# Performance work log

Hardware: AMD Instinct MI355X
Metric: run time of the kernel (lower is better)

The kernel has to match this reference:

```python
import jax, jax.numpy as jnp
import numpy as np

TEMP = 0.07
LAMBDA_INFONCE = 1.0
LAMBDA_NTXENT = 0.5
EPS = 1e-8

B, S, H, C = 32, 2048, 1024, 5


def _l2norm(x):
    # F.normalize-style row L2 normalization
    n = jnp.sqrt(jnp.sum(x * x, axis=1, keepdims=True))
    return x / jnp.maximum(n, 1e-12)


def _proj(x, W1, b1, W2, b2):
    h = jax.nn.relu(x @ W1 + b1)
    return _l2norm(h @ W2 + b2)


def setup_inputs() -> dict:
    key = jax.random.key(0)
    ks = jax.random.split(key, 12)
    sc1 = 1.0 / np.sqrt(H)
    sc2 = 1.0 / np.sqrt(H // 2)
    sc3 = 1.0 / np.sqrt(2 * H)
    return {
        "span_features": jax.random.normal(ks[0], (B, S, H), jnp.float32),
        "aspect_logits": jax.random.normal(ks[1], (B, S, C), jnp.float32),
        "opinion_logits": jax.random.normal(ks[2], (B, S, C), jnp.float32),
        "sentiment_labels": jax.random.randint(ks[3], (B,), 0, 3),
        "Wa1": jax.random.normal(ks[4], (H, H // 2), jnp.float32) * sc1,
        "ba1": jnp.zeros((H // 2,), jnp.float32),
        "Wa2": jax.random.normal(ks[5], (H // 2, 128), jnp.float32) * sc2,
        "ba2": jnp.zeros((128,), jnp.float32),
        "Wo1": jax.random.normal(ks[6], (H, H // 2), jnp.float32) * sc1,
        "bo1": jnp.zeros((H // 2,), jnp.float32),
        "Wo2": jax.random.normal(ks[7], (H // 2, 128), jnp.float32) * sc2,
        "bo2": jnp.zeros((128,), jnp.float32),
        "Ws1": jax.random.normal(ks[8], (2 * H, H), jnp.float32) * sc3,
        "bs1": jnp.zeros((H,), jnp.float32),
        "Ws2": jax.random.normal(ks[9], (H, 256), jnp.float32) * sc1,
        "bs2": jnp.zeros((256,), jnp.float32),
    }


def _pool(span_features, logits):
    # attention pooling: softmax over seq of summed non-O class logits
    w = jax.nn.softmax(logits[:, :, 1:].sum(axis=-1), axis=-1)  # [B, S]
    return jnp.einsum("bsh,bs->bh", span_features, w)  # [B, H]


def _infonce(a, o, labels):
    n = a.shape[0]
    sim = (a @ o.T) / TEMP  # [B, B]
    same = labels[:, None] == labels[None, :]
    eye = jnp.eye(n, dtype=a.dtype)
    pos_mask = eye + 0.5 * (same & (eye == 0)).astype(a.dtype)
    exp_sim = jnp.exp(sim)
    return -jnp.mean(jnp.log((exp_sim * pos_mask).sum(1) / exp_sim.sum(1) + EPS))


def _ntxent(s, labels):
    n = s.shape[0]
    s = _l2norm(s)
    sim = (s @ s.T) / TEMP
    same = (labels[:, None] == labels[None, :]).astype(s.dtype)
    mask = same - jnp.eye(n, dtype=s.dtype)
    exp_sim = jnp.exp(sim)
    pos = (exp_sim * mask).sum(1)
    neg = (exp_sim * (1.0 - mask)).sum(1)
    pos_count = mask.sum(1)
    has_pos = pos_count > 0
    row = jnp.where(has_pos,
                    -jnp.log(pos / (pos + neg) + EPS) / jnp.maximum(pos_count, 1.0),
                    0.0)
    return row.sum() / jnp.maximum(has_pos.sum(), 1).astype(s.dtype)


def reference(span_features, aspect_logits, opinion_logits, sentiment_labels,
              Wa1, ba1, Wa2, ba2, Wo1, bo1, Wo2, bo2, Ws1, bs1, Ws2, bs2):
    a_emb = _pool(span_features, aspect_logits)   # [B, H]
    o_emb = _pool(span_features, opinion_logits)  # [B, H]
    a_proj = _proj(a_emb, Wa1, ba1, Wa2, ba2)     # [B, 128]
    o_proj = _proj(o_emb, Wo1, bo1, Wo2, bo2)     # [B, 128]
    infonce = _infonce(a_proj, o_proj, sentiment_labels)
    s_proj = _proj(jnp.concatenate([a_emb, o_emb], axis=-1), Ws1, bs1, Ws2, bs2)
    ntxent = _ntxent(s_proj, sentiment_labels)
    # generation_embeddings is None -> cross_modal_loss = 0
    return LAMBDA_INFONCE * infonce + LAMBDA_NTXENT * ntxent
```

## Files before the change

kernel.cpp:

```cpp
#include <hip/hip_runtime.h>
#include <hip/hip_bf16.h>

#define BB 32
#define SS 2048
#define HH 1024
#define CC 5
#define TEMP_INV (1.0f/0.07f)

__global__ __launch_bounds__(256) void pool_weights(const float* __restrict__ alog,
                             const float* __restrict__ olog,
                             float* __restrict__ w_a,
                             float* __restrict__ w_o) {
    int b = blockIdx.x >> 1;
    int which = blockIdx.x & 1;
    const float* lg = which ? olog : alog;
    float* wout = which ? w_o : w_a;
    __shared__ float raw[SS * CC];
    __shared__ float sl[SS];
    __shared__ float red[256];
    int t = threadIdx.x;
    const float4* src = (const float4*)(lg + (size_t)b * SS * CC);
    float4* dst = (float4*)raw;
    #pragma unroll 4
    for (int i = t; i < SS * CC / 4; i += 256) dst[i] = src[i];
    __syncthreads();
    for (int s = t; s < SS; s += 256) {
        int base = s * 5;
        sl[s] = raw[base + 1] + raw[base + 2] + raw[base + 3] + raw[base + 4];
    }
    __syncthreads();
    float m = -1e30f;
    for (int s = t; s < SS; s += 256) m = fmaxf(m, sl[s]);
    red[t] = m;
    __syncthreads();
    for (int o = 128; o > 0; o >>= 1) {
        if (t < o) red[t] = fmaxf(red[t], red[t + o]);
        __syncthreads();
    }
    m = red[0];
    __syncthreads();
    float sum = 0.f;
    for (int s = t; s < SS; s += 256) {
        float e = expf(sl[s] - m);
        sl[s] = e;
        sum += e;
    }
    red[t] = sum;
    __syncthreads();
    for (int o = 128; o > 0; o >>= 1) {
        if (t < o) red[t] += red[t + o];
        __syncthreads();
    }
    float inv = 1.0f / red[0];
    for (int s = t; s < SS; s += 256) wout[(size_t)b * SS + s] = sl[s] * inv;
}

__global__ __launch_bounds__(256) void pool_partial(const float* __restrict__ span,
                             const float* __restrict__ w_a,
                             const float* __restrict__ w_o,
                             float* __restrict__ part_a,
                             float* __restrict__ part_o) {
    int b = blockIdx.x >> 5;
    int chunk = blockIdx.x & 31;
    int t = threadIdx.x;
    __shared__ float wa[64], wo[64];
    int s0 = chunk * 64;
    if (t < 64) {
        wa[t] = w_a[(size_t)b * SS + s0 + t];
        wo[t] = w_o[(size_t)b * SS + s0 + t];
    }
    __syncthreads();
    const float4* sp = (const float4*)span + ((size_t)b * SS + s0) * (HH / 4) + t;
    float4 aa = {0.f, 0.f, 0.f, 0.f};
    float4 oo = {0.f, 0.f, 0.f, 0.f};
    #pragma unroll 16
    for (int ss = 0; ss < 64; ++ss) {
        float4 v = sp[(size_t)ss * (HH / 4)];
        float fa = wa[ss], fo = wo[ss];
        aa.x += v.x * fa; aa.y += v.y * fa; aa.z += v.z * fa; aa.w += v.w * fa;
        oo.x += v.x * fo; oo.y += v.y * fo; oo.z += v.z * fo; oo.w += v.w * fo;
    }
    size_t idx = ((size_t)chunk * BB + b) * HH + (size_t)t * 4;
    *(float4*)(part_a + idx) = aa;
    *(float4*)(part_o + idx) = oo;
}

__global__ __launch_bounds__(256) void pool_reduce(const float* __restrict__ part_a,
                            const float* __restrict__ part_o,
                            float* __restrict__ a_emb,
                            float* __restrict__ o_emb) {
    int gid = blockIdx.x * 256 + threadIdx.x;
    int which = gid >> 15;
    int r = gid & 32767;
    const float* p = which ? part_o : part_a;
    float s = 0.f;
    #pragma unroll
    for (int c = 0; c < 32; ++c) s += p[(size_t)c * 32768 + r];
    (which ? o_emb : a_emb)[r] = s;
}

__global__ __launch_bounds__(512) void gemm1_all(const float* __restrict__ a_emb, const float* __restrict__ o_emb,
                          const float* __restrict__ Wa1, const float* __restrict__ Wo1,
                          const float* __restrict__ Ws1,
                          float* __restrict__ p1_a, float* __restrict__ p1_o,
                          float* __restrict__ p1_s) {
    int bid = blockIdx.x;
    const float* xp; const float* W; float* part; int N, kb, jb;
    if (bid < 64) {
        jb = bid & 7; kb = bid >> 3; N = 512; W = Wa1; part = p1_a;
        xp = a_emb + kb * 128;
    } else if (bid < 128) {
        int r = bid - 64;
        jb = r & 7; kb = r >> 3; N = 512; W = Wo1; part = p1_o;
        xp = o_emb + kb * 128;
    } else {
        int r = bid - 128;
        jb = r & 15; kb = r >> 4; N = 1024; W = Ws1; part = p1_s;
        int kk0 = kb * 128;
        xp = (kk0 < 1024) ? (a_emb + kk0) : (o_emb + (kk0 - 1024));
    }
    int k0 = kb * 128;
    __shared__ float xs[32][128];
    int t = threadIdx.x;
    #pragma unroll
    for (int i = 0; i < 2; ++i) {
        int f = t + i * 512;
        int b = f >> 5;
        int kk = (f & 31) * 4;
        *(float4*)(&xs[b][kk]) = *(const float4*)(xp + (size_t)b * HH + kk);
    }
    __syncthreads();
    int jl = t & 63, bg = t >> 6;
    int j = jb * 64 + jl;
    float acc[4] = {0.f, 0.f, 0.f, 0.f};
    const float* Wp = W + (size_t)k0 * N + j;
    #pragma unroll 8
    for (int k = 0; k < 128; k += 4) {
        float w0 = Wp[(size_t)(k + 0) * N];
        float w1 = Wp[(size_t)(k + 1) * N];
        float w2 = Wp[(size_t)(k + 2) * N];
        float w3 = Wp[(size_t)(k + 3) * N];
        #pragma unroll
        for (int bi = 0; bi < 4; ++bi) {
            float4 xv = *(const float4*)(&xs[bg * 4 + bi][k]);
            acc[bi] += xv.x * w0 + xv.y * w1 + xv.z * w2 + xv.w * w3;
        }
    }
    float* pp = part + (size_t)kb * 32 * N + j;
    #pragma unroll
    for (int bi = 0; bi < 4; ++bi)
        pp[(size_t)(bg * 4 + bi) * N] = acc[bi];
}

__global__ __launch_bounds__(512) void layer2_all(const float* __restrict__ p1_a, const float* __restrict__ ba1,
                           const float* __restrict__ Wa2, const float* __restrict__ ba2,
                           const float* __restrict__ p1_o, const float* __restrict__ bo1,
                           const float* __restrict__ Wo2, const float* __restrict__ bo2,
                           const float* __restrict__ p1_s, const float* __restrict__ bs1,
                           const float* __restrict__ Ws2, const float* __restrict__ bs2,
                           float* __restrict__ a_proj, float* __restrict__ o_proj,
                           float* __restrict__ s_proj) {
    __shared__ float x[1024];
    __shared__ float red[512];
    int bid = blockIdx.x;
    int t = threadIdx.x;
    if (bid < 64) {
        int which = bid >> 5;
        int b = bid & 31;
        const float* part = which ? p1_o : p1_a;
        const float* b1 = which ? bo1 : ba1;
        const float* W2 = which ? Wo2 : Wa2;
        const float* b2 = which ? bo2 : ba2;
        float* out = (which ? o_proj : a_proj) + (size_t)b * 128;
        {
            float s = b1[t];
            #pragma unroll
            for (int kb = 0; kb < 8; ++kb) s += part[(size_t)kb * 32 * 512 + (size_t)b * 512 + t];
            x[t] = fmaxf(s, 0.f);
        }
        __syncthreads();
        int jj = t & 127, kh = t >> 7;
        int kbase = kh * 128;
        const float* Wc = W2 + (size_t)kbase * 128 + jj;
        float acc = 0.f;
        #pragma unroll 16
        for (int kk = 0; kk < 128; ++kk)
            acc += x[kbase + kk] * Wc[(size_t)kk * 128];
        if (kh == 0) acc += b2[jj];
        red[t] = acc;
        __syncthreads();
        float tot = 0.f;
        if (t < 128) tot = red[t] + red[t + 128] + red[t + 256] + red[t + 384];
        __syncthreads();
        if (t < 128) red[t] = tot * tot;
        __syncthreads();
        for (int o = 64; o > 0; o >>= 1) {
            if (t < o) red[t] += red[t + o];
            __syncthreads();
        }
        float n = fmaxf(sqrtf(red[0]), 1e-12f);
        if (t < 128) out[t] = tot / n;
    } else {
        int b = bid - 64;
        for (int j = t; j < 1024; j += 512) {
            float s = bs1[j];
            #pragma unroll
            for (int kb = 0; kb < 16; ++kb) s += p1_s[(size_t)kb * 32 * 1024 + (size_t)b * 1024 + j];
            x[j] = fmaxf(s, 0.f);
        }
        __syncthreads();
        int jj = t & 255, kh = t >> 8;
        int kbase = kh * 512;
        const float* Wc = Ws2 + (size_t)kbase * 256 + jj;
        float acc = 0.f;
        #pragma unroll 16
        for (int kk = 0; kk < 512; ++kk)
            acc += x[kbase + kk] * Wc[(size_t)kk * 256];
        if (kh == 0) acc += bs2[jj];
        red[t] = acc;
        __syncthreads();
        float tot = 0.f;
        if (t < 256) tot = red[t] + red[t + 256];
        __syncthreads();
        if (t < 256) red[t] = tot * tot;
        __syncthreads();
        for (int o = 128; o > 0; o >>= 1) {
            if (t < o) red[t] += red[t + o];
            __syncthreads();
        }
        float n = fmaxf(sqrtf(red[0]), 1e-12f);
        if (t < 256) s_proj[(size_t)b * 256 + t] = tot / n;
    }
}

__global__ __launch_bounds__(256) void loss_rows(const float* __restrict__ a_proj,
                            const float* __restrict__ o_proj,
                            const float* __restrict__ s_proj,
                            const int* __restrict__ labels,
                            float* __restrict__ rowbuf) {
    int i = blockIdx.x;
    __shared__ __align__(16) float spn[BB][260];
    __shared__ __align__(16) float opn[BB][132];
    __shared__ __align__(16) float api[128];
    __shared__ float invn[BB];
    __shared__ float jv[BB][5];
    __shared__ int lab[BB];
    int t = threadIdx.x;
    for (int q = t; q < 2048; q += 256) {
        int r = q >> 6, c = (q & 63) << 2;
        *(float4*)&spn[r][c] = *(const float4*)(s_proj + r * 256 + c);
    }
    for (int q = t; q < 1024; q += 256) {
        int r = q >> 5, c = (q & 31) << 2;
        *(float4*)&opn[r][c] = *(const float4*)(o_proj + r * 128 + c);
    }
    if (t < 32) *(float4*)&api[t * 4] = *(const float4*)(a_proj + (size_t)i * 128 + t * 4);
    if (t < BB) lab[t] = labels[t];
    __syncthreads();

    int r = t >> 3, l = t & 7;
    {
        float ssq = 0.f;
        #pragma unroll
        for (int q = 0; q < 8; ++q) {
            int c = (q * 8 + l) * 4;
            float4 v = *(float4*)&spn[r][c];
            ssq += v.x * v.x + v.y * v.y + v.z * v.z + v.w * v.w;
        }
        ssq += __shfl_xor(ssq, 1, 8);
        ssq += __shfl_xor(ssq, 2, 8);
        ssq += __shfl_xor(ssq, 4, 8);
        if (l == 0) invn[r] = 1.0f / fmaxf(sqrtf(ssq), 1e-12f);
    }
    __syncthreads();
    {
        float s = invn[r];
        #pragma unroll
        for (int q = 0; q < 8; ++q) {
            int c = (q * 8 + l) * 4;
            float4 v = *(float4*)&spn[r][c];
            v.x *= s; v.y *= s; v.z *= s; v.w *= s;
            *(float4*)&spn[r][c] = v;
        }
    }
    __syncthreads();

    int j = r;
    float dot = 0.f;
    #pragma unroll
    for (int q = 0; q < 4; ++q) {
        int c = (q * 8 + l) * 4;
        float4 av = *(float4*)&api[c];
        float4 ov = *(float4*)&opn[j][c];
        dot += av.x * ov.x + av.y * ov.y + av.z * ov.z + av.w * ov.w;
    }
    float dn = 0.f;
    #pragma unroll
    for (int q = 0; q < 8; ++q) {
        int c = (q * 8 + l) * 4;
        float4 si = *(float4*)&spn[i][c];
        float4 sj = *(float4*)&spn[j][c];
        dn += si.x * sj.x + si.y * sj.y + si.z * sj.z + si.w * sj.w;
    }
    dot += __shfl_xor(dot, 1, 8); dot += __shfl_xor(dot, 2, 8); dot += __shfl_xor(dot, 4, 8);
    dn  += __shfl_xor(dn, 1, 8);  dn  += __shfl_xor(dn, 2, 8);  dn  += __shfl_xor(dn, 4, 8);
    if (l == 0) {
        float e = expf(dot * TEMP_INV);
        float maskv = (i == j) ? 1.0f : ((lab[i] == lab[j]) ? 0.5f : 0.0f);
        float en = expf(dn * TEMP_INV);
        float mnt = (lab[i] == lab[j]) ? ((i == j) ? 0.f : 1.f) : 0.f;
        jv[j][0] = e * maskv;
        jv[j][1] = e;
        jv[j][2] = en * mnt;
        jv[j][3] = en * (1.f - mnt);
        jv[j][4] = mnt;
    }
    __syncthreads();
    if (t < 32) {
        float num = jv[t][0], den = jv[t][1], pos = jv[t][2], neg = jv[t][3], pc = jv[t][4];
        for (int m = 16; m > 0; m >>= 1) {
            num += __shfl_xor(num, m, 32);
            den += __shfl_xor(den, m, 32);
            pos += __shfl_xor(pos, m, 32);
            neg += __shfl_xor(neg, m, 32);
            pc  += __shfl_xor(pc, m, 32);
        }
        if (t == 0) {
            rowbuf[i] = -logf(num / den + 1e-8f);
            bool has = pc > 0.f;
            rowbuf[32 + i] = has ? (-logf(pos / (pos + neg) + 1e-8f) / fmaxf(pc, 1.0f)) : 0.f;
            rowbuf[64 + i] = has ? 1.f : 0.f;
        }
    }
}

__global__ __launch_bounds__(64) void loss_final(const float* __restrict__ rowbuf,
                                                 float* __restrict__ out) {
    if (threadIdx.x == 0) {
        float inf = 0.f, nt = 0.f;
        int h = 0;
        #pragma unroll
        for (int q = 0; q < 32; ++q) {
            inf += rowbuf[q];
            nt += rowbuf[32 + q];
            h += (rowbuf[64 + q] > 0.5f) ? 1 : 0;
        }
        inf /= (float)BB;
        nt /= (float)(h > 0 ? h : 1);
        out[0] = 1.0f * inf + 0.5f * nt;
    }
}

extern "C" void kernel_launch(void* const* d_in, const int* in_sizes, int n_in,
                              void* d_out, int out_size, void* d_ws, size_t ws_size,
                              hipStream_t stream) {
    const float* span  = (const float*)d_in[0];
    const float* alog  = (const float*)d_in[1];
    const float* olog  = (const float*)d_in[2];
    const int*   labs  = (const int*)d_in[3];
    const float* Wa1   = (const float*)d_in[4];
    const float* ba1   = (const float*)d_in[5];
    const float* Wa2   = (const float*)d_in[6];
    const float* ba2   = (const float*)d_in[7];
    const float* Wo1   = (const float*)d_in[8];
    const float* bo1   = (const float*)d_in[9];
    const float* Wo2   = (const float*)d_in[10];
    const float* bo2   = (const float*)d_in[11];
    const float* Ws1   = (const float*)d_in[12];
    const float* bs1   = (const float*)d_in[13];
    const float* Ws2   = (const float*)d_in[14];
    const float* bs2   = (const float*)d_in[15];

    float* ws = (float*)d_ws;
    float* w_a    = ws;
    float* w_o    = ws + 65536;
    float* part_a = ws + 131072;
    float* part_o = ws + 1179648;
    float* a_emb  = ws + 2228224;
    float* o_emb  = ws + 2260992;
    float* p1_a   = ws + 2293760;
    float* p1_o   = ws + 2424832;
    float* p1_s   = ws + 2555904;
    float* a_proj = ws + 3080192;
    float* o_proj = ws + 3084288;
    float* s_proj = ws + 3088384;
    float* rowbuf = ws + 3096576;

    hipLaunchKernelGGL(pool_weights, dim3(64), dim3(256), 0, stream, alog, olog, w_a, w_o);
    hipLaunchKernelGGL(pool_partial, dim3(1024), dim3(256), 0, stream,
                       span, w_a, w_o, part_a, part_o);
    hipLaunchKernelGGL(pool_reduce, dim3(256), dim3(256), 0, stream,
                       part_a, part_o, a_emb, o_emb);
    hipLaunchKernelGGL(gemm1_all, dim3(384), dim3(512), 0, stream,
                       a_emb, o_emb, Wa1, Wo1, Ws1, p1_a, p1_o, p1_s);
    hipLaunchKernelGGL(layer2_all, dim3(96), dim3(512), 0, stream,
                       p1_a, ba1, Wa2, ba2, p1_o, bo1, Wo2, bo2,
                       p1_s, bs1, Ws2, bs2, a_proj, o_proj, s_proj);
    hipLaunchKernelGGL(loss_rows, dim3(32), dim3(256), 0, stream,
                       a_proj, o_proj, s_proj, labs, rowbuf);
    hipLaunchKernelGGL(loss_final, dim3(1), dim3(64), 0, stream,
                       rowbuf, (float*)d_out);
}
```

Before: 447.7 us.

## Retile layer-1 GEMM with float4 weight loads and fuse final loss reduction

The first-layer GEMM now splits K into chunks of 64 instead of 128, giving twice as many K partials. Each of 256 threads computes a 4x4 output tile using float4 weight loads. The second-layer kernel reads these extra partials and uses float4 weights, a float4 shared-memory tree reduction and a warp-shuffle norm. The separate loss_final launch is removed: the last loss_rows block, found through an atomic counter, does the final sum. This saves one launch and widens memory accesses, at the cost of doubling the partial-sum traffic and adding atomic/fence logic.

```diff
diff --git a/kernel.cpp b/kernel.cpp
--- a/kernel.cpp
+++ b/kernel.cpp
@@ -10,7 +10,9 @@
 __global__ __launch_bounds__(256) void pool_weights(const float* __restrict__ alog,
                              const float* __restrict__ olog,
                              float* __restrict__ w_a,
-                             float* __restrict__ w_o) {
+                             float* __restrict__ w_o,
+                             int* __restrict__ counter) {
+    if (blockIdx.x == 0 && threadIdx.x == 0) *counter = 0;
     int b = blockIdx.x >> 1;
     int which = blockIdx.x & 1;
     const float* lg = which ? olog : alog;
@@ -99,57 +101,57 @@
     (which ? o_emb : a_emb)[r] = s;
 }
 
-__global__ __launch_bounds__(512) void gemm1_all(const float* __restrict__ a_emb, const float* __restrict__ o_emb,
+__global__ __launch_bounds__(256) void gemm1_all(const float* __restrict__ a_emb, const float* __restrict__ o_emb,
                           const float* __restrict__ Wa1, const float* __restrict__ Wo1,
                           const float* __restrict__ Ws1,
                           float* __restrict__ p1_a, float* __restrict__ p1_o,
                           float* __restrict__ p1_s) {
     int bid = blockIdx.x;
-    const float* xp; const float* W; float* part; int N, kb, jb;
+    const float* xp; const float* W; float* part; int N, kb, jt;
     if (bid < 64) {
-        jb = bid & 7; kb = bid >> 3; N = 512; W = Wa1; part = p1_a;
-        xp = a_emb + kb * 128;
+        jt = bid & 3; kb = bid >> 2; N = 512; W = Wa1; part = p1_a;
+        xp = a_emb + kb * 64;
     } else if (bid < 128) {
         int r = bid - 64;
-        jb = r & 7; kb = r >> 3; N = 512; W = Wo1; part = p1_o;
-        xp = o_emb + kb * 128;
+        jt = r & 3; kb = r >> 2; N = 512; W = Wo1; part = p1_o;
+        xp = o_emb + kb * 64;
     } else {
         int r = bid - 128;
-        jb = r & 15; kb = r >> 4; N = 1024; W = Ws1; part = p1_s;
-        int kk0 = kb * 128;
+        jt = r & 7; kb = r >> 3; N = 1024; W = Ws1; part = p1_s;
+        int kk0 = kb * 64;
         xp = (kk0 < 1024) ? (a_emb + kk0) : (o_emb + (kk0 - 1024));
     }
-    int k0 = kb * 128;
-    __shared__ float xs[32][128];
+    int k0 = kb * 64;
+    __shared__ float xs[32][64];
     int t = threadIdx.x;
     #pragma unroll
     for (int i = 0; i < 2; ++i) {
-        int f = t + i * 512;
-        int b = f >> 5;
-        int kk = (f & 31) * 4;
+        int f = t + i * 256;
+        int b = f >> 4;
+        int kk = (f & 15) << 2;
         *(float4*)(&xs[b][kk]) = *(const float4*)(xp + (size_t)b * HH + kk);
     }
     __syncthreads();
-    int jl = t & 63, bg = t >> 6;
-    int j = jb * 64 + jl;
-    float acc[4] = {0.f, 0.f, 0.f, 0.f};
+    int jq = t & 31, bg = t >> 5;
+    int j = jt * 128 + jq * 4;
+    float4 a0 = {0,0,0,0}, a1 = {0,0,0,0}, a2 = {0,0,0,0}, a3 = {0,0,0,0};
     const float* Wp = W + (size_t)k0 * N + j;
+    int b0 = bg * 4;
     #pragma unroll 8
-    for (int k = 0; k < 128; k += 4) {
-        float w0 = Wp[(size_t)(k + 0) * N];
-        float w1 = Wp[(size_t)(k + 1) * N];
-        float w2 = Wp[(size_t)(k + 2) * N];
-        float w3 = Wp[(size_t)(k + 3) * N];
-        #pragma unroll
-        for (int bi = 0; bi < 4; ++bi) {
-            float4 xv = *(const float4*)(&xs[bg * 4 + bi][k]);
-            acc[bi] += xv.x * w0 + xv.y * w1 + xv.z * w2 + xv.w * w3;
-        }
+    for (int k = 0; k < 64; ++k) {
+        float4 w4 = *(const float4*)(Wp + (size_t)k * N);
+        float x0 = xs[b0 + 0][k], x1 = xs[b0 + 1][k];
+        float x2 = xs[b0 + 2][k], x3 = xs[b0 + 3][k];
+        a0.x += w4.x * x0; a0.y += w4.y * x0; a0.z += w4.z * x0; a0.w += w4.w * x0;
+        a1.x += w4.x * x1; a1.y += w4.y * x1; a1.z += w4.z * x1; a1.w += w4.w * x1;
+        a2.x += w4.x * x2; a2.y += w4.y * x2; a2.z += w4.z * x2; a2.w += w4.w * x2;
+        a3.x += w4.x * x3; a3.y += w4.y * x3; a3.z += w4.z * x3; a3.w += w4.w * x3;
     }
     float* pp = part + (size_t)kb * 32 * N + j;
-    #pragma unroll
-    for (int bi = 0; bi < 4; ++bi)
-        pp[(size_t)(bg * 4 + bi) * N] = acc[bi];
+    *(float4*)(pp + (size_t)(b0 + 0) * N) = a0;
+    *(float4*)(pp + (size_t)(b0 + 1) * N) = a1;
+    *(float4*)(pp + (size_t)(b0 + 2) * N) = a2;
+    *(float4*)(pp + (size_t)(b0 + 3) * N) = a3;
 }
 
 __global__ __launch_bounds__(512) void layer2_all(const float* __restrict__ p1_a, const float* __restrict__ ba1,
@@ -161,7 +163,7 @@
                            float* __restrict__ a_proj, float* __restrict__ o_proj,
                            float* __restrict__ s_proj) {
     __shared__ float x[1024];
-    __shared__ float red[512];
+    __shared__ float4 red4[512];
     int bid = blockIdx.x;
     int t = threadIdx.x;
     if (bid < 64) {
@@ -175,61 +177,81 @@
         {
             float s = b1[t];
             #pragma unroll
-            for (int kb = 0; kb < 8; ++kb) s += part[(size_t)kb * 32 * 512 + (size_t)b * 512 + t];
+            for (int kb = 0; kb < 16; ++kb) s += part[(size_t)kb * 16384 + (size_t)b * 512 + t];
             x[t] = fmaxf(s, 0.f);
         }
         __syncthreads();
-        int jj = t & 127, kh = t >> 7;
-        int kbase = kh * 128;
-        const float* Wc = W2 + (size_t)kbase * 128 + jj;
-        float acc = 0.f;
-        #pragma unroll 16
-        for (int kk = 0; kk < 128; ++kk)
-            acc += x[kbase + kk] * Wc[(size_t)kk * 128];
-        if (kh == 0) acc += b2[jj];
-        red[t] = acc;
-        __syncthreads();
-        float tot = 0.f;
-        if (t < 128) tot = red[t] + red[t + 128] + red[t + 256] + red[t + 384];
-        __syncthreads();
-        if (t < 128) red[t] = tot * tot;
-        __syncthreads();
-        for (int o = 64; o > 0; o >>= 1) {
-            if (t < o) red[t] += red[t + o];
+        int jq = t & 31, kh = t >> 5;
+        const float* Wc = W2 + (size_t)kh * 32 * 128 + jq * 4;
+        float4 acc = {0,0,0,0};
+        #pragma unroll 8
+        for (int kk = 0; kk < 32; ++kk) {
+            float4 w4 = *(const float4*)(Wc + (size_t)kk * 128);
+            float xv = x[kh * 32 + kk];
+            acc.x += w4.x * xv; acc.y += w4.y * xv; acc.z += w4.z * xv; acc.w += w4.w * xv;
+        }
+        red4[t] = acc;
+        __syncthreads();
+        for (int o = 8; o > 0; o >>= 1) {
+            if (kh < o) {
+                float4 u = red4[kh * 32 + jq], v = red4[(kh + o) * 32 + jq];
+                u.x += v.x; u.y += v.y; u.z += v.z; u.w += v.w;
+                red4[kh * 32 + jq] = u;
+            }
             __syncthreads();
         }
-        float n = fmaxf(sqrtf(red[0]), 1e-12f);
-        if (t < 128) out[t] = tot / n;
+        if (t < 32) {
+            float4 tot = red4[t];
+            float4 bq = *(const float4*)(b2 + t * 4);
+            tot.x += bq.x; tot.y += bq.y; tot.z += bq.z; tot.w += bq.w;
+            float ss = tot.x * tot.x + tot.y * tot.y + tot.z * tot.z + tot.w * tot.w;
+            #pragma unroll
+            for (int m = 16; m > 0; m >>= 1) ss += __shfl_xor(ss, m, 32);
+            float inv = 1.0f / fmaxf(sqrtf(ss), 1e-12f);
+            tot.x *= inv; tot.y *= inv; tot.z *= inv; tot.w *= inv;
+            *(float4*)(out + t * 4) = tot;
+        }
     } else {
         int b = bid - 64;
-        for (int j = t; j < 1024; j += 512) {
+        #pragma unroll
+        for (int i = 0; i < 2; ++i) {
+            int j = t + i * 512;
             float s = bs1[j];
             #pragma unroll
-            for (int kb = 0; kb < 16; ++kb) s += p1_s[(size_t)kb * 32 * 1024 + (size_t)b * 1024 + j];
+            for (int kb = 0; kb < 32; ++kb) s += p1_s[(size_t)kb * 32768 + (size_t)b * 1024 + j];
             x[j] = fmaxf(s, 0.f);
         }
         __syncthreads();
-        int jj = t & 255, kh = t >> 8;
-        int kbase = kh * 512;
-        const float* Wc = Ws2 + (size_t)kbase * 256 + jj;
-        float acc = 0.f;
-        #pragma unroll 16
-        for (int kk = 0; kk < 512; ++kk)
-            acc += x[kbase + kk] * Wc[(size_t)kk * 256];
-        if (kh == 0) acc += bs2[jj];
-        red[t] = acc;
-        __syncthreads();
-        float tot = 0.f;
-        if (t < 256) tot = red[t] + red[t + 256];
-        __syncthreads();
-        if (t < 256) red[t] = tot * tot;
-        __syncthreads();
-        for (int o = 128; o > 0; o >>= 1) {
-            if (t < o) red[t] += red[t + o];
+        int jq = t & 63, kh = t >> 6;
+        const float* Wc = Ws2 + (size_t)kh * 128 * 256 + jq * 4;
+        float4 acc = {0,0,0,0};
+        #pragma unroll 8
+        for (int kk = 0; kk < 128; ++kk) {
+            float4 w4 = *(const float4*)(Wc + (size_t)kk * 256);
+            float xv = x[kh * 128 + kk];
+            acc.x += w4.x * xv; acc.y += w4.y * xv; acc.z += w4.z * xv; acc.w += w4.w * xv;
+        }
+        red4[t] = acc;
+        __syncthreads();
+        for (int o = 4; o > 0; o >>= 1) {
+            if (kh < o) {
+                float4 u = red4[kh * 64 + jq], v = red4[(kh + o) * 64 + jq];
+                u.x += v.x; u.y += v.y; u.z += v.z; u.w += v.w;
+                red4[kh * 64 + jq] = u;
+            }
             __syncthreads();
         }
-        float n = fmaxf(sqrtf(red[0]), 1e-12f);
-        if (t < 256) s_proj[(size_t)b * 256 + t] = tot / n;
+        if (t < 64) {
+            float4 tot = red4[t];
+            float4 bq = *(const float4*)(bs2 + t * 4);
+            tot.x += bq.x; tot.y += bq.y; tot.z += bq.z; tot.w += bq.w;
+            float ss = tot.x * tot.x + tot.y * tot.y + tot.z * tot.z + tot.w * tot.w;
+            #pragma unroll
+            for (int m = 32; m > 0; m >>= 1) ss += __shfl_xor(ss, m, 64);
+            float inv = 1.0f / fmaxf(sqrtf(ss), 1e-12f);
+            tot.x *= inv; tot.y *= inv; tot.z *= inv; tot.w *= inv;
+            *(float4*)(s_proj + (size_t)b * 256 + t * 4) = tot;
+        }
     }
 }
 
@@ -237,7 +259,9 @@
                             const float* __restrict__ o_proj,
                             const float* __restrict__ s_proj,
                             const int* __restrict__ labels,
-                            float* __restrict__ rowbuf) {
+                            float* __restrict__ rowbuf,
+                            int* __restrict__ counter,
+                            float* __restrict__ out) {
     int i = blockIdx.x;
     __shared__ __align__(16) float spn[BB][260];
     __shared__ __align__(16) float opn[BB][132];
@@ -332,22 +356,23 @@
             rowbuf[64 + i] = has ? 1.f : 0.f;
         }
     }
-}
-
-__global__ __launch_bounds__(64) void loss_final(const float* __restrict__ rowbuf,
-                                                 float* __restrict__ out) {
-    if (threadIdx.x == 0) {
-        float inf = 0.f, nt = 0.f;
-        int h = 0;
-        #pragma unroll
-        for (int q = 0; q < 32; ++q) {
-            inf += rowbuf[q];
-            nt += rowbuf[32 + q];
-            h += (rowbuf[64 + q] > 0.5f) ? 1 : 0;
-        }
-        inf /= (float)BB;
-        nt /= (float)(h > 0 ? h : 1);
-        out[0] = 1.0f * inf + 0.5f * nt;
+    __syncthreads();
+    if (t == 0) {
+        __threadfence();
+        int old = __hip_atomic_fetch_add(counter, 1, __ATOMIC_ACQ_REL, __HIP_MEMORY_SCOPE_AGENT);
+        if (old == 31) {
+            float inf = 0.f, nt = 0.f;
+            int h = 0;
+            #pragma unroll
+            for (int q = 0; q < 32; ++q) {
+                inf += __hip_atomic_load(&rowbuf[q], __ATOMIC_RELAXED, __HIP_MEMORY_SCOPE_AGENT);
+                nt  += __hip_atomic_load(&rowbuf[32 + q], __ATOMIC_RELAXED, __HIP_MEMORY_SCOPE_AGENT);
+                h   += (__hip_atomic_load(&rowbuf[64 + q], __ATOMIC_RELAXED, __HIP_MEMORY_SCOPE_AGENT) > 0.5f) ? 1 : 0;
+            }
+            inf /= (float)BB;
+            nt /= (float)(h > 0 ? h : 1);
+            out[0] = 1.0f * inf + 0.5f * nt;
+        }
     }
 }
 
@@ -379,25 +404,25 @@
     float* a_emb  = ws + 2228224;
     float* o_emb  = ws + 2260992;
     float* p1_a   = ws + 2293760;
-    float* p1_o   = ws + 2424832;
-    float* p1_s   = ws + 2555904;
-    float* a_proj = ws + 3080192;
-    float* o_proj = ws + 3084288;
-    float* s_proj = ws + 3088384;
-    float* rowbuf = ws + 3096576;
-
-    hipLaunchKernelGGL(pool_weights, dim3(64), dim3(256), 0, stream, alog, olog, w_a, w_o);
+    float* p1_o   = ws + 2555904;
+    float* p1_s   = ws + 2818048;
+    float* a_proj = ws + 3866624;
+    float* o_proj = ws + 3870720;
+    float* s_proj = ws + 3874816;
+    float* rowbuf = ws + 3883008;
+    int*   counter = (int*)(ws + 3883104);
+
+    hipLaunchKernelGGL(pool_weights, dim3(64), dim3(256), 0, stream,
+                       alog, olog, w_a, w_o, counter);
     hipLaunchKernelGGL(pool_partial, dim3(1024), dim3(256), 0, stream,
                        span, w_a, w_o, part_a, part_o);
     hipLaunchKernelGGL(pool_reduce, dim3(256), dim3(256), 0, stream,
                        part_a, part_o, a_emb, o_emb);
-    hipLaunchKernelGGL(gemm1_all, dim3(384), dim3(512), 0, stream,
+    hipLaunchKernelGGL(gemm1_all, dim3(384), dim3(256), 0, stream,
                        a_emb, o_emb, Wa1, Wo1, Ws1, p1_a, p1_o, p1_s);
     hipLaunchKernelGGL(layer2_all, dim3(96), dim3(512), 0, stream,
                        p1_a, ba1, Wa2, ba2, p1_o, bo1, Wo2, bo2,
                        p1_s, bs1, Ws2, bs2, a_proj, o_proj, s_proj);
     hipLaunchKernelGGL(loss_rows, dim3(32), dim3(256), 0, stream,
-                       a_proj, o_proj, s_proj, labs, rowbuf);
-    hipLaunchKernelGGL(loss_final, dim3(1), dim3(64), 0, stream,
-                       rowbuf, (float*)d_out);
-}
+                       a_proj, o_proj, s_proj, labs, rowbuf, counter, (float*)d_out);
+}
```

Result: no change. 454.6 us (+1.5%).
